# Kernel tuning notes

Measured on AMD Instinct MI355X. Metric: run time of the kernel, lower is better.

The kernel has to match this reference:

```python
import jax, jax.numpy as jnp
import numpy as np

N, E = 50000, 800000
F_IN, HID, CLS, K = 128, 128, 40, 4


def setup_inputs() -> dict:
    key = jax.random.key(0)
    ks = jax.random.split(key, 6)
    x = jax.random.normal(ks[0], (N, F_IN), jnp.float32)
    edge_src = jax.random.randint(ks[1], (E,), 0, N, jnp.int32)
    edge_dst = jax.random.randint(ks[2], (E,), 0, N, jnp.int32)
    glorot = lambda k, sh, fan: jax.random.normal(k, sh, jnp.float32) * np.float32(1.0 / np.sqrt(fan))
    W0 = glorot(ks[3], (K, F_IN, HID), F_IN)
    W1 = glorot(ks[4], (K, HID, HID), HID)
    W2 = glorot(ks[5], (K, HID, CLS), HID)
    b0 = jnp.zeros((HID,), jnp.float32)
    b1 = jnp.zeros((HID,), jnp.float32)
    b2 = jnp.zeros((CLS,), jnp.float32)
    return dict(x=x, edge_src=edge_src, edge_dst=edge_dst,
                W0=W0, b0=b0, W1=W1, b1=b1, W2=W2, b2=b2)


def _cheb_edge_norm(edge_src, edge_dst, n):
    # PyG ChebConv 'sym' norm with lambda_max=2: scaled Laplacian
    # L_hat = 2L/lambda_max - I = -D^{-1/2} A D^{-1/2}  (diagonal is exactly 0)
    ones = jnp.ones(edge_src.shape[0], jnp.float32)
    deg = jax.ops.segment_sum(ones, edge_src, num_segments=n)
    dinv = jnp.where(deg > 0, jax.lax.rsqrt(jnp.maximum(deg, 1.0)), 0.0)
    return -dinv[edge_src] * dinv[edge_dst]  # [E]


def _cheb_conv(x, edge_src, edge_dst, w_norm, W, b, n):
    # Chebyshev recurrence: Tx0 = x, Tx1 = L_hat x, Tx_k = 2 L_hat Tx_{k-1} - Tx_{k-2}
    def lhat(t):  # SpMM: out[dst] += w * t[src]
        return jax.ops.segment_sum(t[edge_src] * w_norm[:, None], edge_dst, num_segments=n)

    Tx0 = x
    out = Tx0 @ W[0]
    Tx1 = lhat(Tx0)
    out = out + Tx1 @ W[1]
    for k in range(2, W.shape[0]):
        Tx2 = 2.0 * lhat(Tx1) - Tx0
        out = out + Tx2 @ W[k]
        Tx0, Tx1 = Tx1, Tx2
    return out + b


def reference(x, edge_src, edge_dst, W0, b0, W1, b1, W2, b2):
    n = x.shape[0]
    w_norm = _cheb_edge_norm(edge_src, edge_dst, n)
    h = x
    x1 = h
    for W, b in ((W0, b0), (W1, b1), (W2, b2)):
        x1 = _cheb_conv(h, edge_src, edge_dst, w_norm, W, b, n)
        h = jax.nn.relu(x1)  # dropout(p=0.6) is identity in eval mode
    # original returns log_softmax of the LAST conv's pre-activation x1
    return jax.nn.log_softmax(x1, axis=1)
```

## Files before the change

### kernel.cpp

```cpp
#include <hip/hip_runtime.h>
#include <math.h>

#define NN 50000
#define NE 800000
#define FDIM 128
#define CLS 40
#define AW 512
#define ZW 256

#define BSH 7
#define BINS 128
#define NBUK 391
#define NB_E 196
#define EUNITS 1024
#define U4 (NE / 4)
#define HL (NBUK * NB_E)
#define SCAN_CHUNK 2048
#define NB_S ((HL + SCAN_CHUNK - 1) / SCAN_CHUNK)
#define BSLACK 4096

typedef __attribute__((ext_vector_type(8))) short short8v;
typedef __attribute__((ext_vector_type(8))) unsigned short ushort8v;
typedef __attribute__((ext_vector_type(4))) float f32x4;

__device__ inline float b2f(unsigned short u) {
    union { unsigned int i; float f; } v; v.i = ((unsigned)u) << 16; return v.f;
}
__device__ inline unsigned short f2b(float f) {
    unsigned int x = __float_as_uint(f);
    unsigned int r = (x + 0x7fffu + ((x >> 16) & 1u)) >> 16;
    return (unsigned short)r;
}

#define NB_CVT  3125
#define NB_WH   256
#define NB_WZ   128

__global__ __launch_bounds__(256) void prep_k(
        const int4* __restrict__ esrc4, const int4* __restrict__ edst4,
        int* degi, int* __restrict__ hist,
        const float* __restrict__ x, unsigned short* __restrict__ Ab,
        const float* __restrict__ W0, const float* __restrict__ W1,
        const float* __restrict__ W2,
        unsigned short* __restrict__ Wt0, unsigned short* __restrict__ Wt1,
        unsigned short* __restrict__ Wz) {
    int b = blockIdx.x;
    int tid = threadIdx.x;
    if (b < NB_E) {
        __shared__ int lcnt[NBUK];
        for (int i = tid; i < NBUK; i += 256) lcnt[i] = 0;
        __syncthreads();
        #pragma unroll
        for (int it = 0; it < 4; it++) {
            int u = b * EUNITS + it * 256 + tid;
            if (u < U4) {
                int4 s = esrc4[u], d = edst4[u];
                atomicAdd(&degi[s.x], 1); atomicAdd(&degi[s.y], 1);
                atomicAdd(&degi[s.z], 1); atomicAdd(&degi[s.w], 1);
                atomicAdd(&lcnt[d.x >> BSH], 1); atomicAdd(&lcnt[d.y >> BSH], 1);
                atomicAdd(&lcnt[d.z >> BSH], 1); atomicAdd(&lcnt[d.w >> BSH], 1);
            }
        }
        __syncthreads();
        for (int i = tid; i < NBUK; i += 256) hist[i * NB_E + b] = lcnt[i];
    } else if (b < NB_E + NB_CVT) {
        int i = (b - NB_E) * 256 + tid;
        int row = i >> 4, cg = i & 15;
        const float4* xp = (const float4*)(x + (size_t)row * FDIM + cg * 8);
        float4 v0 = xp[0], v1 = xp[1];
        ushort8v r;
        r[0] = f2b(v0.x); r[1] = f2b(v0.y); r[2] = f2b(v0.z); r[3] = f2b(v0.w);
        r[4] = f2b(v1.x); r[5] = f2b(v1.y); r[6] = f2b(v1.z); r[7] = f2b(v1.w);
        *(ushort8v*)(Ab + (size_t)row * AW + cg * 8) = r;
    } else if (b < NB_E + NB_CVT + 2 * NB_WH) {
        int wi = b - NB_E - NB_CVT;
        const float* W = (wi < NB_WH) ? W0 : W1;
        unsigned short* Wfm = (wi < NB_WH) ? Wt0 : Wt1;
        int i = (wi % NB_WH) * 256 + tid;
        int j = i & 7, l = (i >> 3) & 63, kcl = (i >> 9) & 3, nt = (i >> 11) & 7, c = i >> 14;
        int r = kcl * 32 + (l >> 4) * 8 + j;
        int col = nt * 16 + (l & 15);
        Wfm[i] = f2b(W[((size_t)c * 128 + r) * 128 + col]);
    } else {
        int i = (b - NB_E - NB_CVT - 2 * NB_WH) * 256 + tid;
        int j = i & 7, l = (i >> 3) & 63, kcl = (i >> 9) & 3, nt = (i >> 11) & 7, half = (i >> 14) & 1;
        int k = kcl * 32 + (l >> 4) * 8 + j;
        int col = half * 128 + nt * 16 + (l & 15);
        int kcheb = col >> 6, cc = col & 63;
        float v = (cc < CLS) ? W2[((size_t)kcheb * 128 + k) * CLS + cc] : 0.0f;
        Wz[i] = f2b(v);
    }
}


__global__ void scanA_k(const int* __restrict__ hist, int* __restrict__ bsum) {
    __shared__ int lds[256];
    int base = blockIdx.x * SCAN_CHUNK;
    int s = 0;
    for (int j = threadIdx.x; j < SCAN_CHUNK; j += 256) {
        int i = base + j;
        if (i < HL) s += hist[i];
    }
    lds[threadIdx.x] = s;
    __syncthreads();
    for (int off = 128; off > 0; off >>= 1) {
        if (threadIdx.x < off) lds[threadIdx.x] += lds[threadIdx.x + off];
        __syncthreads();
    }
    if (threadIdx.x == 0) bsum[blockIdx.x] = lds[0];
}

__global__ void scanB_k(int* bsum, int* scanned) {
    if (threadIdx.x == 0 && blockIdx.x == 0) {
        int run = 0;
        for (int b = 0; b < NB_S; b++) { int t = bsum[b]; bsum[b] = run; run += t; }
        scanned[HL] = run;
    }
}

__global__ void scanC_k(const int* __restrict__ hist, const int* __restrict__ bsum,
                        int* __restrict__ scanned) {
    __shared__ int lds[256];
    int base = blockIdx.x * SCAN_CHUNK + threadIdx.x * 8;
    int v[8];
    int s = 0;
    #pragma unroll
    for (int j = 0; j < 8; j++) {
        int i = base + j;
        v[j] = (i < HL) ? hist[i] : 0;
        s += v[j];
    }
    lds[threadIdx.x] = s;
    __syncthreads();
    for (int off = 1; off < 256; off <<= 1) {
        int t = (threadIdx.x >= (unsigned)off) ? lds[threadIdx.x - off] : 0;
        __syncthreads();
        lds[threadIdx.x] += t;
        __syncthreads();
    }
    int incl = lds[threadIdx.x];
    int excl = incl - s;
    int run = bsum[blockIdx.x] + excl;
    #pragma unroll
    for (int j = 0; j < 8; j++) {
        int i = base + j;
        if (i < HL) scanned[i] = run;
        run += v[j];
    }
}


__global__ __launch_bounds__(256) void part_k(const int4* __restrict__ esrc4,
                                              const int4* __restrict__ edst4,
                                              const int* __restrict__ scanned,
                                              int* __restrict__ ebuf) {
    __shared__ int lcnt[NBUK];
    int b = blockIdx.x;
    int tid = threadIdx.x;
    for (int i = tid; i < NBUK; i += 256) lcnt[i] = 0;
    __syncthreads();
    #pragma unroll
    for (int it = 0; it < 4; it++) {
        int u = b * EUNITS + it * 256 + tid;
        if (u < U4) {
            int4 s = esrc4[u], d = edst4[u];
            int dd[4] = {d.x, d.y, d.z, d.w};
            int ss[4] = {s.x, s.y, s.z, s.w};
            #pragma unroll
            for (int j = 0; j < 4; j++) {
                int bin = dd[j] >> BSH;
                int r = atomicAdd(&lcnt[bin], 1);
                int pos = scanned[bin * NB_E + b] + r;
                ebuf[pos] = ((dd[j] & (BINS - 1)) << 16) | ss[j];
            }
        }
    }
}


__global__ __launch_bounds__(256) void bsort_k(const int* __restrict__ scanned,
                                               const int* __restrict__ ebuf,
                                               int* __restrict__ ews,
                                               int* __restrict__ rp,
                                               int* __restrict__ rpe) {
    __shared__ int cnt[BINS], excl[BINS], rnk[BINS];
    int b = blockIdx.x;
    int tid = threadIdx.x;
    int s0b = scanned[b * NB_E];
    int s1b = scanned[(b + 1) * NB_E];
    if (tid < BINS) { cnt[tid] = 0; rnk[tid] = 0; }
    __syncthreads();
    for (int e = s0b + tid; e < s1b; e += 256)
        atomicAdd(&cnt[ebuf[e] >> 16], 1);
    __syncthreads();
    if (tid == 0) {
        int run = 0;
        for (int i = 0; i < BINS; i++) { excl[i] = run; run += (cnt[i] + 31) & ~31; }
    }
    __syncthreads();
    int abase = (s0b + b * BSLACK + 31) & ~31;
    if (tid < BINS) {
        int node = b * BINS + tid;
        if (node < NN) {
            rp[node]  = abase + excl[tid];
            rpe[node] = abase + excl[tid] + ((cnt[tid] + 31) & ~31);
        }
    }
    for (int e = s0b + tid; e < s1b; e += 256) {
        int pk = ebuf[e];
        int low = pk >> 16;
        int pos = abase + excl[low] + atomicAdd(&rnk[low], 1);
        ews[pos] = pk & 0xFFFF;
    }
    for (int i = tid; i < BINS * 32; i += 256) {
        int bin = i >> 5;
        int off = cnt[bin] + (i & 31);
        if (off < ((cnt[bin] + 31) & ~31))
            ews[abase + excl[bin] + off] = NN;
    }
}


__global__ void dinv_k(const int* __restrict__ degi, float* __restrict__ dinv) {
    int i = blockIdx.x * blockDim.x + threadIdx.x;
    if (i < NN) {
        int d = degi[i];
        dinv[i] = (d > 0) ? rsqrtf((float)d) : 0.0f;
    } else if (i == NN) {
        dinv[i] = 0.0f;
    }
}


template <bool CHEB>
__global__ __launch_bounds__(256) void spmm_k(const unsigned short* __restrict__ inp,
                                              const unsigned short* __restrict__ prevp,
                                              unsigned short* __restrict__ outp,
                                              const int* __restrict__ rp,
                                              const int* __restrict__ rpe,
                                              const int* __restrict__ ews,
                                              const float* __restrict__ dinv) {
    int row = blockIdx.x * 4 + (threadIdx.x >> 6);
    int lane = threadIdx.x & 63;
    int slot = lane >> 4, ln = lane & 15;
    int e0 = rp[row], e1 = rpe[row];
    float dvr = dinv[row];
    float acc[8] = {0.f, 0.f, 0.f, 0.f, 0.f, 0.f, 0.f, 0.f};
    for (int e = e0; e < e1; e += 16) {
        int4 s4 = *(const int4*)&ews[e + slot * 4];
        ushort8v t0 = *(const ushort8v*)(inp + (size_t)s4.x * AW + ln * 8);
        ushort8v t1 = *(const ushort8v*)(inp + (size_t)s4.y * AW + ln * 8);
        ushort8v t2 = *(const ushort8v*)(inp + (size_t)s4.z * AW + ln * 8);
        ushort8v t3 = *(const ushort8v*)(inp + (size_t)s4.w * AW + ln * 8);
        float w0 = -dinv[s4.x] * dvr, w1 = -dinv[s4.y] * dvr;
        float w2 = -dinv[s4.z] * dvr, w3 = -dinv[s4.w] * dvr;
        #pragma unroll
        for (int j = 0; j < 8; j++)
            acc[j] += w0 * b2f(t0[j]) + w1 * b2f(t1[j]) + w2 * b2f(t2[j]) + w3 * b2f(t3[j]);
    }
    #pragma unroll
    for (int j = 0; j < 8; j++) {
        acc[j] += __shfl_xor(acc[j], 16);
        acc[j] += __shfl_xor(acc[j], 32);
    }
    if (slot == 0) {
        ushort8v r;
        if (CHEB) {
            ushort8v p = *(const ushort8v*)(prevp + (size_t)row * AW + ln * 8);
            #pragma unroll
            for (int j = 0; j < 8; j++) r[j] = f2b(2.f * acc[j] - b2f(p[j]));
        } else {
            #pragma unroll
            for (int j = 0; j < 8; j++) r[j] = f2b(acc[j]);
        }
        *(ushort8v*)(outp + (size_t)row * AW + ln * 8) = r;
    }
}


template <int MODE>
__global__ __launch_bounds__(256) void spmm64_k(const unsigned short* __restrict__ gsrc,
                                                const unsigned short* __restrict__ zadd,
                                                const unsigned short* __restrict__ bsub,
                                                unsigned short* __restrict__ wout,
                                                float* __restrict__ fout,
                                                const int* __restrict__ rp,
                                                const int* __restrict__ rpe,
                                                const int* __restrict__ ews,
                                                const float* __restrict__ dinv) {
    constexpr int GS = (MODE == 0) ? ZW : 64;
    constexpr float SC = (MODE == 2) ? 1.0f : 2.0f;
    int row = blockIdx.x * 4 + (threadIdx.x >> 6);
    int lane = threadIdx.x & 63;
    int slot = lane >> 3, ln = lane & 7;
    int e0 = rp[row], e1 = rpe[row];
    float dvr = dinv[row];
    float acc[8] = {0.f, 0.f, 0.f, 0.f, 0.f, 0.f, 0.f, 0.f};
    for (int e = e0; e < e1; e += 32) {
        int4 s4 = *(const int4*)&ews[e + slot * 4];
        ushort8v t0 = *(const ushort8v*)(gsrc + (size_t)s4.x * GS + ln * 8);
        ushort8v t1 = *(const ushort8v*)(gsrc + (size_t)s4.y * GS + ln * 8);
        ushort8v t2 = *(const ushort8v*)(gsrc + (size_t)s4.z * GS + ln * 8);
        ushort8v t3 = *(const ushort8v*)(gsrc + (size_t)s4.w * GS + ln * 8);
        float w0 = -dinv[s4.x] * dvr, w1 = -dinv[s4.y] * dvr;
        float w2 = -dinv[s4.z] * dvr, w3 = -dinv[s4.w] * dvr;
        #pragma unroll
        for (int j = 0; j < 8; j++)
            acc[j] += w0 * b2f(t0[j]) + w1 * b2f(t1[j]) + w2 * b2f(t2[j]) + w3 * b2f(t3[j]);
    }
    #pragma unroll
    for (int j = 0; j < 8; j++) {
        acc[j] += __shfl_xor(acc[j], 8);
        acc[j] += __shfl_xor(acc[j], 16);
        acc[j] += __shfl_xor(acc[j], 32);
    }
    if (slot != 0) return;
    ushort8v zv = *(const ushort8v*)(zadd + (size_t)row * ZW + ln * 8);
    float v[8];
    if (MODE == 0) {
        #pragma unroll
        for (int j = 0; j < 8; j++) v[j] = b2f(zv[j]) + SC * acc[j];
    } else {
        constexpr int BS = (MODE == 1) ? ZW : 64;
        ushort8v bv = *(const ushort8v*)(bsub + (size_t)row * BS + ln * 8);
        #pragma unroll
        for (int j = 0; j < 8; j++) v[j] = b2f(zv[j]) + SC * acc[j] - b2f(bv[j]);
    }
    if (MODE < 2) {
        ushort8v r;
        #pragma unroll
        for (int j = 0; j < 8; j++) r[j] = f2b(v[j]);
        *(ushort8v*)(wout + (size_t)row * 64 + ln * 8) = r;
    } else {
        float m = -INFINITY;
        #pragma unroll
        for (int j = 0; j < 8; j++) if (ln * 8 + j < CLS) m = fmaxf(m, v[j]);
        #pragma unroll
        for (int off = 4; off >= 1; off >>= 1) m = fmaxf(m, __shfl_xor(m, off));
        float s = 0.f;
        #pragma unroll
        for (int j = 0; j < 8; j++) if (ln * 8 + j < CLS) s += __expf(v[j] - m);
        #pragma unroll
        for (int off = 4; off >= 1; off >>= 1) s += __shfl_xor(s, off);
        float ls = logf(s) + m;
        #pragma unroll
        for (int j = 0; j < 8; j++) {
            int col = ln * 8 + j;
            if (col < CLS) fout[(size_t)row * CLS + col] = v[j] - ls;
        }
    }
}


__global__ __launch_bounds__(256) void gemm_hid_k(const unsigned short* __restrict__ A,
                                                  const unsigned short* __restrict__ Wfm,
                                                  const float* __restrict__ bias,
                                                  unsigned short* __restrict__ Hout) {
    __shared__ unsigned short Blds[16384];
    int tid = threadIdx.x;
    int w = tid >> 6, lane = tid & 63, ln = lane & 15, gp = lane >> 4;
    int rowbase = blockIdx.x * 64 + w * 16;
    int rowc = rowbase + ln;
    if (rowc >= NN) rowc = NN - 1;
    const unsigned short* Arow = A + (size_t)rowc * AW + gp * 8;

    f32x4 acc[8];
    #pragma unroll
    for (int i = 0; i < 8; i++) acc[i] = (f32x4){0.f, 0.f, 0.f, 0.f};

    short8v acur[4], anxt[4];
    #pragma unroll
    for (int kcl = 0; kcl < 4; kcl++) acur[kcl] = *(const short8v*)(Arow + kcl * 32);
    {
        const ushort8v* g = (const ushort8v*)Wfm;
        ushort8v* s = (ushort8v*)Blds;
        #pragma unroll
        for (int i = 0; i < 8; i++) s[tid + i * 256] = g[tid + i * 256];
    }
    __syncthreads();

    for (int c = 0; c < 4; c++) {
        if (c < 3) {
            #pragma unroll
            for (int kcl = 0; kcl < 4; kcl++)
                anxt[kcl] = *(const short8v*)(Arow + (c + 1) * 128 + kcl * 32);
        }
        #pragma unroll
        for (int kcl = 0; kcl < 4; kcl++) {
            #pragma unroll
            for (int nt = 0; nt < 8; nt++) {
                short8v b = *(const short8v*)&Blds[((nt * 4 + kcl) * 64 + lane) * 8];
                acc[nt] = __builtin_amdgcn_mfma_f32_16x16x32_bf16(acur[kcl], b, acc[nt], 0, 0, 0);
            }
        }
        if (c < 3) {
            __syncthreads();
            const ushort8v* g = (const ushort8v*)(Wfm + (c + 1) * 16384);
            ushort8v* s = (ushort8v*)Blds;
            #pragma unroll
            for (int i = 0; i < 8; i++) s[tid + i * 256] = g[tid + i * 256];
            __syncthreads();
            #pragma unroll
            for (int kcl = 0; kcl < 4; kcl++) acur[kcl] = anxt[kcl];
        }
    }

    if (rowbase < NN) {
        #pragma unroll
        for (int nt = 0; nt < 8; nt++) {
            int col = nt * 16 + ln;
            float bv = bias[col];
            #pragma unroll
            for (int j = 0; j < 4; j++) {
                int r = rowbase + gp * 4 + j;
                Hout[(size_t)r * AW + col] = f2b(fmaxf(acc[nt][j] + bv, 0.0f));
            }
        }
    }
}


__global__ __launch_bounds__(256) void gemm_z_k(const unsigned short* __restrict__ A,
                                                const unsigned short* __restrict__ Wz,
                                                const float* __restrict__ b2,
                                                unsigned short* __restrict__ Z) {
    __shared__ unsigned short Blds[16384];
    int tid = threadIdx.x;
    int w = tid >> 6, lane = tid & 63, ln = lane & 15, gp = lane >> 4;
    int rowbase = blockIdx.x * 64 + w * 16;
    int rowc = rowbase + ln;
    if (rowc >= NN) rowc = NN - 1;
    const unsigned short* Arow = A + (size_t)rowc * AW + gp * 8;

    short8v af[4];
    #pragma unroll
    for (int kcl = 0; kcl < 4; kcl++) af[kcl] = *(const short8v*)(Arow + kcl * 32);

    for (int half = 0; half < 2; half++) {
        if (half) __syncthreads();
        {
            const ushort8v* g = (const ushort8v*)(Wz + half * 16384);
            ushort8v* s = (ushort8v*)Blds;
            #pragma unroll
            for (int i = 0; i < 8; i++) s[tid + i * 256] = g[tid + i * 256];
        }
        __syncthreads();
        f32x4 acc[8];
        #pragma unroll
        for (int i = 0; i < 8; i++) acc[i] = (f32x4){0.f, 0.f, 0.f, 0.f};
        #pragma unroll
        for (int kcl = 0; kcl < 4; kcl++) {
            #pragma unroll
            for (int nt = 0; nt < 8; nt++) {
                short8v b = *(const short8v*)&Blds[((nt * 4 + kcl) * 64 + lane) * 8];
                acc[nt] = __builtin_amdgcn_mfma_f32_16x16x32_bf16(af[kcl], b, acc[nt], 0, 0, 0);
            }
        }
        if (rowbase < NN) {
            #pragma unroll
            for (int nt = 0; nt < 8; nt++) {
                int col = half * 128 + nt * 16 + ln;
                float bv = (col < CLS) ? b2[col] : 0.0f;
                #pragma unroll
                for (int j = 0; j < 4; j++) {
                    int r = rowbase + gp * 4 + j;
                    Z[(size_t)r * ZW + col] = f2b(acc[nt][j] + bv);
                }
            }
        }
    }
}


extern "C" void kernel_launch(void* const* d_in, const int* in_sizes, int n_in,
                              void* d_out, int out_size, void* d_ws, size_t ws_size,
                              hipStream_t stream) {
    const float* x    = (const float*)d_in[0];
    const int*   esrc = (const int*)d_in[1];
    const int*   edst = (const int*)d_in[2];
    const float* W0   = (const float*)d_in[3];
    const float* b0   = (const float*)d_in[4];
    const float* W1   = (const float*)d_in[5];
    const float* b1   = (const float*)d_in[6];
    const float* W2   = (const float*)d_in[7];
    const float* b2   = (const float*)d_in[8];
    float* out = (float*)d_out;

    char* p = (char*)d_ws;
    auto alloc = [&](size_t bytes) -> void* {
        void* r = (void*)p;
        p += (bytes + 255) & ~(size_t)255;
        return r;
    };
    unsigned short* Abuf = (unsigned short*)alloc((size_t)(NN + 1) * AW * 2);
    unsigned short* Zbuf = (unsigned short*)alloc((size_t)(NN + 1) * ZW * 2);
    unsigned short* B1b  = (unsigned short*)alloc((size_t)(NN + 1) * 64 * 2);
    unsigned short* B2b  = (unsigned short*)alloc((size_t)(NN + 1) * 64 * 2);
    int*   ews     = (int*)alloc((size_t)(NE + NBUK * BSLACK + 64) * 4);
    int*   ebuf    = (int*)alloc((size_t)NE * 4);
    int*   hist    = (int*)alloc((size_t)HL * 4);
    int*   scanned = (int*)alloc((size_t)(HL + 1) * 4);
    int*   bsum    = (int*)alloc(NB_S * 4);
    unsigned short* Wt0 = (unsigned short*)alloc((size_t)128 * AW * 2);
    unsigned short* Wt1 = (unsigned short*)alloc((size_t)128 * AW * 2);
    unsigned short* Wz  = (unsigned short*)alloc((size_t)32768 * 2);
    int*   degi = (int*)alloc(NN * 4);
    int*   rp   = (int*)alloc(NN * 4);
    int*   rpe  = (int*)alloc(NN * 4);
    float* dinv = (float*)alloc((NN + 1) * 4);

    const int TB = 256;

    hipMemsetAsync(degi, 0, NN * 4, stream);
    prep_k<<<NB_E + NB_CVT + 2 * NB_WH + NB_WZ, TB, 0, stream>>>(
        (const int4*)esrc, (const int4*)edst, degi, hist,
        x, Abuf, W0, W1, W2, Wt0, Wt1, Wz);
    scanA_k<<<NB_S, TB, 0, stream>>>(hist, bsum);
    scanB_k<<<1, 64, 0, stream>>>(bsum, scanned);
    scanC_k<<<NB_S, TB, 0, stream>>>(hist, bsum, scanned);
    part_k<<<NB_E, TB, 0, stream>>>((const int4*)esrc, (const int4*)edst, scanned, ebuf);
    bsort_k<<<NBUK, TB, 0, stream>>>(scanned, ebuf, ews, rp, rpe);
    dinv_k<<<(NN + 1 + TB - 1) / TB, TB, 0, stream>>>(degi, dinv);

    int gSpmm = (NN + 3) / 4;
    int gGemm = (NN + 63) / 64;

    unsigned short* s0 = Abuf + 0 * 128;
    unsigned short* s1 = Abuf + 1 * 128;
    unsigned short* s2 = Abuf + 2 * 128;
    unsigned short* s3 = Abuf + 3 * 128;

    for (int l = 0; l < 2; l++) {
        spmm_k<false><<<gSpmm, TB, 0, stream>>>(s0, nullptr, s1, rp, rpe, ews, dinv);
        spmm_k<true><<<gSpmm, TB, 0, stream>>>(s1, s0, s2, rp, rpe, ews, dinv);
        spmm_k<true><<<gSpmm, TB, 0, stream>>>(s2, s1, s3, rp, rpe, ews, dinv);
        const unsigned short* Wt = (l == 0) ? Wt0 : Wt1;
        const float* bl = (l == 0) ? b0 : b1;
        gemm_hid_k<<<gGemm, TB, 0, stream>>>(Abuf, Wt, bl, Abuf);
    }

    gemm_z_k<<<gGemm, TB, 0, stream>>>(Abuf, Wz, b2, Zbuf);
    spmm64_k<0><<<gSpmm, TB, 0, stream>>>(Zbuf + 192, Zbuf + 128, nullptr,
                                          B2b, nullptr, rp, rpe, ews, dinv);
    spmm64_k<1><<<gSpmm, TB, 0, stream>>>(B2b, Zbuf + 64, Zbuf + 192,
                                          B1b, nullptr, rp, rpe, ews, dinv);
    spmm64_k<2><<<gSpmm, TB, 0, stream>>>(B1b, Zbuf, B2b,
                                          nullptr, out, rp, rpe, ews, dinv);
}
```

Measured before the change: 391.4 us.

## Compute degrees via binned source partition and compact last Z slice

Replaces global atomic degree counting with per-block LDS histograms over source bins. Source indices are then partitioned into a compact buffer and counted per bin in a new kernel that also writes dinv. Separately, gemm_z writes the slice consumed by the first spmm64 into a dense 64-wide buffer, so that gather reads rows with stride 64 instead of 256. The scan grows to twice the histogram length and partitioning does extra atomics and writes, adding preprocessing work.

```diff
diff --git a/kernel.cpp b/kernel.cpp
--- a/kernel.cpp
+++ b/kernel.cpp
@@ -15,8 +15,9 @@
 #define EUNITS 1024
 #define U4 (NE / 4)
 #define HL (NBUK * NB_E)
+#define HL2 (2 * HL)
 #define SCAN_CHUNK 2048
-#define NB_S ((HL + SCAN_CHUNK - 1) / SCAN_CHUNK)
+#define NB_S ((HL2 + SCAN_CHUNK - 1) / SCAN_CHUNK)
 #define BSLACK 4096
 
 typedef __attribute__((ext_vector_type(8))) short short8v;
@@ -38,7 +39,7 @@
 
 __global__ __launch_bounds__(256) void prep_k(
         const int4* __restrict__ esrc4, const int4* __restrict__ edst4,
-        int* degi, int* __restrict__ hist,
+        int* __restrict__ hist,
         const float* __restrict__ x, unsigned short* __restrict__ Ab,
         const float* __restrict__ W0, const float* __restrict__ W1,
         const float* __restrict__ W2,
@@ -47,22 +48,25 @@
     int b = blockIdx.x;
     int tid = threadIdx.x;
     if (b < NB_E) {
-        __shared__ int lcnt[NBUK];
-        for (int i = tid; i < NBUK; i += 256) lcnt[i] = 0;
+        __shared__ int lcd[NBUK], lcs[NBUK];
+        for (int i = tid; i < NBUK; i += 256) { lcd[i] = 0; lcs[i] = 0; }
         __syncthreads();
         #pragma unroll
         for (int it = 0; it < 4; it++) {
             int u = b * EUNITS + it * 256 + tid;
             if (u < U4) {
                 int4 s = esrc4[u], d = edst4[u];
-                atomicAdd(&degi[s.x], 1); atomicAdd(&degi[s.y], 1);
-                atomicAdd(&degi[s.z], 1); atomicAdd(&degi[s.w], 1);
-                atomicAdd(&lcnt[d.x >> BSH], 1); atomicAdd(&lcnt[d.y >> BSH], 1);
-                atomicAdd(&lcnt[d.z >> BSH], 1); atomicAdd(&lcnt[d.w >> BSH], 1);
+                atomicAdd(&lcd[d.x >> BSH], 1); atomicAdd(&lcd[d.y >> BSH], 1);
+                atomicAdd(&lcd[d.z >> BSH], 1); atomicAdd(&lcd[d.w >> BSH], 1);
+                atomicAdd(&lcs[s.x >> BSH], 1); atomicAdd(&lcs[s.y >> BSH], 1);
+                atomicAdd(&lcs[s.z >> BSH], 1); atomicAdd(&lcs[s.w >> BSH], 1);
             }
         }
         __syncthreads();
-        for (int i = tid; i < NBUK; i += 256) hist[i * NB_E + b] = lcnt[i];
+        for (int i = tid; i < NBUK; i += 256) {
+            hist[i * NB_E + b] = lcd[i];
+            hist[HL + i * NB_E + b] = lcs[i];
+        }
     } else if (b < NB_E + NB_CVT) {
         int i = (b - NB_E) * 256 + tid;
         int row = i >> 4, cg = i & 15;
@@ -99,7 +103,7 @@
     int s = 0;
     for (int j = threadIdx.x; j < SCAN_CHUNK; j += 256) {
         int i = base + j;
-        if (i < HL) s += hist[i];
+        if (i < HL2) s += hist[i];
     }
     lds[threadIdx.x] = s;
     __syncthreads();
@@ -114,7 +118,7 @@
     if (threadIdx.x == 0 && blockIdx.x == 0) {
         int run = 0;
         for (int b = 0; b < NB_S; b++) { int t = bsum[b]; bsum[b] = run; run += t; }
-        scanned[HL] = run;
+        scanned[HL2] = run;
     }
 }
 
@@ -127,7 +131,7 @@
     #pragma unroll
     for (int j = 0; j < 8; j++) {
         int i = base + j;
-        v[j] = (i < HL) ? hist[i] : 0;
+        v[j] = (i < HL2) ? hist[i] : 0;
         s += v[j];
     }
     lds[threadIdx.x] = s;
@@ -144,7 +148,7 @@
     #pragma unroll
     for (int j = 0; j < 8; j++) {
         int i = base + j;
-        if (i < HL) scanned[i] = run;
+        if (i < HL2) scanned[i] = run;
         run += v[j];
     }
 }
@@ -153,11 +157,12 @@
 __global__ __launch_bounds__(256) void part_k(const int4* __restrict__ esrc4,
                                               const int4* __restrict__ edst4,
                                               const int* __restrict__ scanned,
-                                              int* __restrict__ ebuf) {
-    __shared__ int lcnt[NBUK];
+                                              int* __restrict__ ebuf,
+                                              unsigned short* __restrict__ sbuf) {
+    __shared__ int lcd[NBUK], lcs[NBUK];
     int b = blockIdx.x;
     int tid = threadIdx.x;
-    for (int i = tid; i < NBUK; i += 256) lcnt[i] = 0;
+    for (int i = tid; i < NBUK; i += 256) { lcd[i] = 0; lcs[i] = 0; }
     __syncthreads();
     #pragma unroll
     for (int it = 0; it < 4; it++) {
@@ -169,12 +174,38 @@
             #pragma unroll
             for (int j = 0; j < 4; j++) {
                 int bin = dd[j] >> BSH;
-                int r = atomicAdd(&lcnt[bin], 1);
-                int pos = scanned[bin * NB_E + b] + r;
-                ebuf[pos] = ((dd[j] & (BINS - 1)) << 16) | ss[j];
+                int r = atomicAdd(&lcd[bin], 1);
+                ebuf[scanned[bin * NB_E + b] + r] = ((dd[j] & (BINS - 1)) << 16) | ss[j];
+                int sbin = ss[j] >> BSH;
+                int r2 = atomicAdd(&lcs[sbin], 1);
+                sbuf[scanned[HL + sbin * NB_E + b] + r2 - NE] = (unsigned short)(ss[j] & (BINS - 1));
             }
         }
     }
+}
+
+
+__global__ __launch_bounds__(256) void degcnt_k(const int* __restrict__ scanned,
+                                                const unsigned short* __restrict__ sbuf,
+                                                float* __restrict__ dinv) {
+    __shared__ int cnt[BINS];
+    int b = blockIdx.x;
+    int tid = threadIdx.x;
+    int s0 = scanned[HL + b * NB_E] - NE;
+    int s1 = scanned[HL + (b + 1) * NB_E] - NE;
+    if (tid < BINS) cnt[tid] = 0;
+    __syncthreads();
+    for (int e = s0 + tid; e < s1; e += 256)
+        atomicAdd(&cnt[sbuf[e]], 1);
+    __syncthreads();
+    if (tid < BINS) {
+        int node = b * BINS + tid;
+        if (node < NN) {
+            int d = cnt[tid];
+            dinv[node] = (d > 0) ? rsqrtf((float)d) : 0.0f;
+        }
+    }
+    if (b == 0 && tid == 255) dinv[NN] = 0.0f;
 }
 
 
@@ -217,17 +248,6 @@
         int off = cnt[bin] + (i & 31);
         if (off < ((cnt[bin] + 31) & ~31))
             ews[abase + excl[bin] + off] = NN;
-    }
-}
-
-
-__global__ void dinv_k(const int* __restrict__ degi, float* __restrict__ dinv) {
-    int i = blockIdx.x * blockDim.x + threadIdx.x;
-    if (i < NN) {
-        int d = degi[i];
-        dinv[i] = (d > 0) ? rsqrtf((float)d) : 0.0f;
-    } else if (i == NN) {
-        dinv[i] = 0.0f;
     }
 }
 
@@ -288,7 +308,6 @@
                                                 const int* __restrict__ rpe,
                                                 const int* __restrict__ ews,
                                                 const float* __restrict__ dinv) {
-    constexpr int GS = (MODE == 0) ? ZW : 64;
     constexpr float SC = (MODE == 2) ? 1.0f : 2.0f;
     int row = blockIdx.x * 4 + (threadIdx.x >> 6);
     int lane = threadIdx.x & 63;
@@ -298,10 +317,10 @@
     float acc[8] = {0.f, 0.f, 0.f, 0.f, 0.f, 0.f, 0.f, 0.f};
     for (int e = e0; e < e1; e += 32) {
         int4 s4 = *(const int4*)&ews[e + slot * 4];
-        ushort8v t0 = *(const ushort8v*)(gsrc + (size_t)s4.x * GS + ln * 8);
-        ushort8v t1 = *(const ushort8v*)(gsrc + (size_t)s4.y * GS + ln * 8);
-        ushort8v t2 = *(const ushort8v*)(gsrc + (size_t)s4.z * GS + ln * 8);
-        ushort8v t3 = *(const ushort8v*)(gsrc + (size_t)s4.w * GS + ln * 8);
+        ushort8v t0 = *(const ushort8v*)(gsrc + (size_t)s4.x * 64 + ln * 8);
+        ushort8v t1 = *(const ushort8v*)(gsrc + (size_t)s4.y * 64 + ln * 8);
+        ushort8v t2 = *(const ushort8v*)(gsrc + (size_t)s4.z * 64 + ln * 8);
+        ushort8v t3 = *(const ushort8v*)(gsrc + (size_t)s4.w * 64 + ln * 8);
         float w0 = -dinv[s4.x] * dvr, w1 = -dinv[s4.y] * dvr;
         float w2 = -dinv[s4.z] * dvr, w3 = -dinv[s4.w] * dvr;
         #pragma unroll
@@ -423,7 +442,8 @@
 __global__ __launch_bounds__(256) void gemm_z_k(const unsigned short* __restrict__ A,
                                                 const unsigned short* __restrict__ Wz,
                                                 const float* __restrict__ b2,
-                                                unsigned short* __restrict__ Z) {
+                                                unsigned short* __restrict__ Z,
+                                                unsigned short* __restrict__ B3c) {
     __shared__ unsigned short Blds[16384];
     int tid = threadIdx.x;
     int w = tid >> 6, lane = tid & 63, ln = lane & 15, gp = lane >> 4;
@@ -464,7 +484,9 @@
                 #pragma unroll
                 for (int j = 0; j < 4; j++) {
                     int r = rowbase + gp * 4 + j;
-                    Z[(size_t)r * ZW + col] = f2b(acc[nt][j] + bv);
+                    unsigned short hv = f2b(acc[nt][j] + bv);
+                    Z[(size_t)r * ZW + col] = hv;
+                    if (half == 1 && nt >= 4) B3c[(size_t)r * 64 + (col - 192)] = hv;
                 }
             }
         }
@@ -493,34 +515,34 @@
         return r;
     };
     unsigned short* Abuf = (unsigned short*)alloc((size_t)(NN + 1) * AW * 2);
-    unsigned short* Zbuf = (unsigned short*)alloc((size_t)(NN + 1) * ZW * 2);
+    unsigned short* Zbuf = (unsigned short*)alloc((size_t)NN * ZW * 2);
     unsigned short* B1b  = (unsigned short*)alloc((size_t)(NN + 1) * 64 * 2);
     unsigned short* B2b  = (unsigned short*)alloc((size_t)(NN + 1) * 64 * 2);
+    unsigned short* B3b  = (unsigned short*)alloc((size_t)(NN + 1) * 64 * 2);
     int*   ews     = (int*)alloc((size_t)(NE + NBUK * BSLACK + 64) * 4);
     int*   ebuf    = (int*)alloc((size_t)NE * 4);
-    int*   hist    = (int*)alloc((size_t)HL * 4);
-    int*   scanned = (int*)alloc((size_t)(HL + 1) * 4);
+    unsigned short* sbuf = (unsigned short*)alloc((size_t)NE * 2);
+    int*   hist    = (int*)alloc((size_t)HL2 * 4);
+    int*   scanned = (int*)alloc((size_t)(HL2 + 1) * 4);
     int*   bsum    = (int*)alloc(NB_S * 4);
     unsigned short* Wt0 = (unsigned short*)alloc((size_t)128 * AW * 2);
     unsigned short* Wt1 = (unsigned short*)alloc((size_t)128 * AW * 2);
     unsigned short* Wz  = (unsigned short*)alloc((size_t)32768 * 2);
-    int*   degi = (int*)alloc(NN * 4);
     int*   rp   = (int*)alloc(NN * 4);
     int*   rpe  = (int*)alloc(NN * 4);
     float* dinv = (float*)alloc((NN + 1) * 4);
 
     const int TB = 256;
 
-    hipMemsetAsync(degi, 0, NN * 4, stream);
     prep_k<<<NB_E + NB_CVT + 2 * NB_WH + NB_WZ, TB, 0, stream>>>(
-        (const int4*)esrc, (const int4*)edst, degi, hist,
+        (const int4*)esrc, (const int4*)edst, hist,
         x, Abuf, W0, W1, W2, Wt0, Wt1, Wz);
     scanA_k<<<NB_S, TB, 0, stream>>>(hist, bsum);
     scanB_k<<<1, 64, 0, stream>>>(bsum, scanned);
     scanC_k<<<NB_S, TB, 0, stream>>>(hist, bsum, scanned);
-    part_k<<<NB_E, TB, 0, stream>>>((const int4*)esrc, (const int4*)edst, scanned, ebuf);
+    part_k<<<NB_E, TB, 0, stream>>>((const int4*)esrc, (const int4*)edst, scanned, ebuf, sbuf);
+    degcnt_k<<<NBUK, TB, 0, stream>>>(scanned, sbuf, dinv);
     bsort_k<<<NBUK, TB, 0, stream>>>(scanned, ebuf, ews, rp, rpe);
-    dinv_k<<<(NN + 1 + TB - 1) / TB, TB, 0, stream>>>(degi, dinv);
 
     int gSpmm = (NN + 3) / 4;
     int gGemm = (NN + 63) / 64;
@@ -539,8 +561,8 @@
         gemm_hid_k<<<gGemm, TB, 0, stream>>>(Abuf, Wt, bl, Abuf);
     }
 
-    gemm_z_k<<<gGemm, TB, 0, stream>>>(Abuf, Wz, b2, Zbuf);
-    spmm64_k<0><<<gSpmm, TB, 0, stream>>>(Zbuf + 192, Zbuf + 128, nullptr,
+    gemm_z_k<<<gGemm, TB, 0, stream>>>(Abuf, Wz, b2, Zbuf, B3b);
+    spmm64_k<0><<<gSpmm, TB, 0, stream>>>(B3b, Zbuf + 128, nullptr,
                                           B2b, nullptr, rp, rpe, ews, dinv);
     spmm64_k<1><<<gSpmm, TB, 0, stream>>>(B2b, Zbuf + 64, Zbuf + 192,
                                           B1b, nullptr, rp, rpe, ews, dinv);
```

Result: faster. 366.2 us (median of 2 runs) (-6.4%).
